# Kernel tuning notes

Measured on AMD Instinct MI355X. Metric: run time of the kernel, lower is better.

Reference implementation:

```python
import jax, jax.numpy as jnp
import numpy as np

B, C, H, W, K = 32, 64, 112, 112, 5


def setup_inputs() -> dict:
    key = jax.random.key(0)
    kx, = jax.random.split(key, 1)
    x = jax.random.uniform(kx, (B, C, H, W), dtype=jnp.float32)
    # parameters per BioNorm.reset_parameters()
    sigma = jnp.ones((C,), jnp.float32)
    pow_p = jnp.full((C,), 2.0, jnp.float32)
    sum_kernel = jnp.full((C, 1, K, K), 1.0 / (K * K), jnp.float32)
    weight = jnp.ones((C,), jnp.float32)
    bias = jnp.zeros((C,), jnp.float32)
    return {"x": x, "sigma": sigma, "pow_p": pow_p, "sum_kernel": sum_kernel,
            "weight": weight, "bias": bias}


def _bionorm(x, sigma, pow_p, sum_kernel, weight, bias):
    s = sigma.reshape(1, -1, 1, 1)
    p = pow_p.reshape(1, -1, 1, 1)
    w = weight.reshape(1, -1, 1, 1)
    b = bias.reshape(1, -1, 1, 1)
    xp = x ** p  # [B,C,H,W]
    # depthwise (grouped) conv, VALID padding -> [B,C,H-K+1,W-K+1]
    sf = jax.lax.conv_general_dilated(
        xp, sum_kernel, window_strides=(1, 1), padding='VALID',
        feature_group_count=C,
        dimension_numbers=('NCHW', 'OIHW', 'NCHW'))
    hks = K // 2
    # replicate-pad back to [B,C,H,W]
    sf = jnp.pad(sf, ((0, 0), (0, 0), (hks, hks), (hks, hks)), mode='edge')
    den = s ** p + sf
    return w * xp / den + b


def reference(x, sigma, pow_p, sum_kernel, weight, bias):
    return _bionorm(x, sigma, pow_p, sum_kernel, weight, bias)
```

## Files before the change

kernel.cpp:

```cpp
#include <hip/hip_runtime.h>


#define Cch 64
#define Hh 112
#define Ww 112
#define TH 28
#define LROWS (TH + 4)
#define ST 116

__global__ __launch_bounds__(256) void bionorm_kernel(
    const float* __restrict__ x, const float* __restrict__ sigma,
    const float* __restrict__ pow_p, const float* __restrict__ sum_kernel,
    const float* __restrict__ weight, const float* __restrict__ bias,
    float* __restrict__ out)
{
    __shared__ float lds[LROWS * ST];

    const int rt  = blockIdx.x;
    const int c   = blockIdx.y;
    const int b   = blockIdx.z;
    const int tid = threadIdx.x;
    const int r0  = rt * TH;

    const float p  = pow_p[c];
    const float sg = sigma[c];
    const float wc = weight[c];
    const float bc = bias[c];
    const bool  p2 = (p == 2.0f);
    const float sp = p2 ? sg * sg : __powf(sg, p);

    float kw[25];
    const float* kp = sum_kernel + c * 25;
    #pragma unroll
    for (int j = 0; j < 25; ++j) kw[j] = kp[j];

    const float* xplane = x + ((size_t)(b * Cch + c)) * Hh * Ww;

    for (int i = tid; i < LROWS * 28; i += 256) {
        int s = i / 28, q = i - s * 28;
        int g = r0 - 2 + s;
        g = g < 0 ? 0 : (g > 111 ? 111 : g);
        const float4 v = *(const float4*)(xplane + g * Ww + q * 4);
        float4 xp;
        if (p2) {
            xp.x = v.x * v.x; xp.y = v.y * v.y;
            xp.z = v.z * v.z; xp.w = v.w * v.w;
        } else {
            xp.x = __powf(v.x, p); xp.y = __powf(v.y, p);
            xp.z = __powf(v.z, p); xp.w = __powf(v.w, p);
        }
        *(float4*)(&lds[s * ST + q * 4]) = xp;
    }
    __syncthreads();

    float* oplane = out + ((size_t)(b * Cch + c)) * Hh * Ww;

    for (int i = tid; i < TH * 28; i += 256) {
        int lr = i / 28, gq = i - lr * 28;
        int r  = r0 + lr;
        int w0 = gq * 4;

        int cr    = r  < 2 ? 2 : (r  > 109 ? 109 : r);
        int cwmin = w0 < 2 ? 2 : (w0 > 109 ? 109 : w0);
        int base  = cwmin - 2;
        int sRow  = cr - r0;

        float S0 = 0.f, S1 = 0.f, S2 = 0.f, S3 = 0.f;
        #pragma unroll
        for (int dy = 0; dy < 5; ++dy) {
            const float* row = &lds[(sRow + dy) * ST + base];
            float rv[8];
            #pragma unroll
            for (int t = 0; t < 8; ++t) rv[t] = row[t];
            #pragma unroll
            for (int dx = 0; dx < 5; ++dx) {
                float kv = kw[dy * 5 + dx];
                S0 = fmaf(kv, rv[dx + 0], S0);
                S1 = fmaf(kv, rv[dx + 1], S1);
                S2 = fmaf(kv, rv[dx + 2], S2);
                S3 = fmaf(kv, rv[dx + 3], S3);
            }
        }

        const float4 xp4 = *(const float4*)(&lds[(lr + 2) * ST + w0]);
        const float xv[4] = {xp4.x, xp4.y, xp4.z, xp4.w};

        float res[4];
        #pragma unroll
        for (int j = 0; j < 4; ++j) {
            int wj  = w0 + j;
            int cwj = wj < 2 ? 2 : (wj > 109 ? 109 : wj);
            int off = cwj - cwmin;
            float s_ = off == 0 ? S0 : off == 1 ? S1 : off == 2 ? S2 : S3;
            res[j] = fmaf(wc * xv[j], __builtin_amdgcn_rcpf(sp + s_), bc);
        }
        float4 o = {res[0], res[1], res[2], res[3]};
        *(float4*)(oplane + r * Ww + w0) = o;
    }
}

extern "C" void kernel_launch(void* const* d_in, const int* in_sizes, int n_in,
                              void* d_out, int out_size, void* d_ws, size_t ws_size,
                              hipStream_t stream) {
    const float* x          = (const float*)d_in[0];
    const float* sigma      = (const float*)d_in[1];
    const float* pow_p      = (const float*)d_in[2];
    const float* sum_kernel = (const float*)d_in[3];
    const float* weight     = (const float*)d_in[4];
    const float* bias       = (const float*)d_in[5];
    float* out = (float*)d_out;

    dim3 grid(4, Cch, 32);
    dim3 block(256);
    bionorm_kernel<<<grid, block, 0, stream>>>(x, sigma, pow_p, sum_kernel,
                                               weight, bias, out);
}
```

Before: 214.7 us.

## Replace LDS tiling with register sliding-window stencil, shuffles, and uniform-kernel box-sum path

The kernel is restructured so each block handles a whole (b,c) plane. Each half-wave takes a 14-row band, and lanes keep a rolling 5-row window of powered values in registers. Horizontal neighbours come from lane shuffles instead of shared memory, and outputs use nontemporal stores. When all 25 kernel weights are equal, a running-sum box filter replaces the 25 FMAs, with a generic fallback for other weights. The intent is to remove LDS traffic, barriers and redundant halo loads, at the cost of fewer blocks and idle lanes (4 of every 32).

```diff
diff --git a/kernel.cpp b/kernel.cpp
--- a/kernel.cpp
+++ b/kernel.cpp
@@ -4,9 +4,8 @@
 #define Cch 64
 #define Hh 112
 #define Ww 112
-#define TH 28
-#define LROWS (TH + 4)
-#define ST 116
+
+typedef float v4f __attribute__((ext_vector_type(4)));
 
 __global__ __launch_bounds__(256) void bionorm_kernel(
     const float* __restrict__ x, const float* __restrict__ sigma,
@@ -14,13 +13,21 @@
     const float* __restrict__ weight, const float* __restrict__ bias,
     float* __restrict__ out)
 {
-    __shared__ float lds[LROWS * ST];
-
-    const int rt  = blockIdx.x;
-    const int c   = blockIdx.y;
-    const int b   = blockIdx.z;
-    const int tid = threadIdx.x;
-    const int r0  = rt * TH;
+    const int c    = blockIdx.x;
+    const int b    = blockIdx.y;
+    const int tid  = threadIdx.x;
+    const int wid  = tid >> 6;
+    const int lane = tid & 63;
+    const int half = lane >> 5;
+    const int li   = lane & 31;
+    if (li >= 28) return;
+
+    const int hb     = wid * 2 + half;
+    const int cstart = (hb == 0) ? 2 : 14 * hb;
+    const int ncent  = (hb == 0 || hb == 7) ? 12 : 14;
+    const int col0   = 4 * li;
+    const bool L0 = (li == 0), L27 = (li == 27);
+    const int laneL = lane - 1, laneR = lane + 1;
 
     const float p  = pow_p[c];
     const float sg = sigma[c];
@@ -29,74 +36,163 @@
     const bool  p2 = (p == 2.0f);
     const float sp = p2 ? sg * sg : __powf(sg, p);
 
+    const float* kp = sum_kernel + c * 25;
     float kw[25];
-    const float* kp = sum_kernel + c * 25;
     #pragma unroll
     for (int j = 0; j < 25; ++j) kw[j] = kp[j];
-
-    const float* xplane = x + ((size_t)(b * Cch + c)) * Hh * Ww;
-
-    for (int i = tid; i < LROWS * 28; i += 256) {
-        int s = i / 28, q = i - s * 28;
-        int g = r0 - 2 + s;
-        g = g < 0 ? 0 : (g > 111 ? 111 : g);
-        const float4 v = *(const float4*)(xplane + g * Ww + q * 4);
-        float4 xp;
-        if (p2) {
-            xp.x = v.x * v.x; xp.y = v.y * v.y;
-            xp.z = v.z * v.z; xp.w = v.w * v.w;
-        } else {
-            xp.x = __powf(v.x, p); xp.y = __powf(v.y, p);
-            xp.z = __powf(v.z, p); xp.w = __powf(v.w, p);
+    bool uni = true;
+    #pragma unroll
+    for (int j = 1; j < 25; ++j) uni = uni && (kw[j] == kw[0]);
+
+    const float* xplane = x + ((size_t)(b * Cch + c)) * (Hh * Ww);
+    float* oplane = out + ((size_t)(b * Cch + c)) * (Hh * Ww);
+
+    #define LOADR(GR) (*(const v4f*)(xplane + (GR) * Ww + col0))
+    const v4f r0 = LOADR(cstart - 2);
+    const v4f r1 = LOADR(cstart - 1);
+    const v4f r2 = LOADR(cstart    );
+    const v4f r3 = LOADR(cstart + 1);
+    v4f pend[2];
+    pend[0] = LOADR(cstart + 2);
+    pend[1] = LOADR(cstart + 3);
+
+    #define P4(V) (p2 ? (V) * (V) \
+        : (v4f){__powf((V).x, p), __powf((V).y, p), __powf((V).z, p), __powf((V).w, p)})
+
+    #define NTST(PTR, VAL) __builtin_nontemporal_store((VAL), (v4f*)(PTR))
+
+    if (uni) {
+        const float k0 = kw[0];
+        v4f xp[5];
+        xp[0] = P4(r0); xp[1] = P4(r1); xp[2] = P4(r2); xp[3] = P4(r3);
+        v4f vs = xp[0] + xp[1] + xp[2] + xp[3];
+
+        #pragma unroll
+        for (int k = 0; k < 14; ++k) {
+            const v4f nw = P4(pend[k & 1]);
+            xp[(k + 4) % 5] = nw;
+            vs += nw;
+            int lr = cstart + 4 + k; if (lr > 111) lr = 111;
+            pend[k & 1] = LOADR(lr);
+
+            const float vs0 = vs.x, vs1 = vs.y, vs2 = vs.z, vs3 = vs.w;
+            const float vL2 = __shfl(vs2, laneL, 64);
+            const float vL3 = __shfl(vs3, laneL, 64);
+            const float vR0 = __shfl(vs0, laneR, 64);
+            const float vR1 = __shfl(vs1, laneR, 64);
+            const float a  = vs0 + vs1 + vs2;
+            float h0 = vL2 + vL3 + a;
+            float h1 = vL3 + a + vs3;
+            float h2 = a + vs3 + vR0;
+            float h3 = (vs1 + vs2 + vs3) + (vR0 + vR1);
+            if (L0)  { h0 = h2; h1 = h2; }
+            if (L27) { h2 = h1; h3 = h1; }
+
+            const float d0 = __builtin_amdgcn_rcpf(fmaf(k0, h0, sp));
+            const float d1 = __builtin_amdgcn_rcpf(fmaf(k0, h1, sp));
+            const float d2 = __builtin_amdgcn_rcpf(fmaf(k0, h2, sp));
+            const float d3 = __builtin_amdgcn_rcpf(fmaf(k0, h3, sp));
+
+            const v4f nm = xp[(k + 2) % 5];
+            const v4f o  = {fmaf(wc * nm.x, d0, bc), fmaf(wc * nm.y, d1, bc),
+                            fmaf(wc * nm.z, d2, bc), fmaf(wc * nm.w, d3, bc)};
+            if (k < ncent)
+                NTST(oplane + (cstart + k) * Ww + col0, o);
+
+            if (hb == 0 && k == 0) {
+                const v4f nA = xp[0], nB = xp[1];
+                NTST(oplane + 0 * Ww + col0,
+                     ((v4f){fmaf(wc*nA.x,d0,bc), fmaf(wc*nA.y,d1,bc),
+                            fmaf(wc*nA.z,d2,bc), fmaf(wc*nA.w,d3,bc)}));
+                NTST(oplane + 1 * Ww + col0,
+                     ((v4f){fmaf(wc*nB.x,d0,bc), fmaf(wc*nB.y,d1,bc),
+                            fmaf(wc*nB.z,d2,bc), fmaf(wc*nB.w,d3,bc)}));
+            }
+            if (hb == 7 && k == 11) {
+                const v4f nA = xp[4];
+                const v4f nB = xp[0];
+                NTST(oplane + 110 * Ww + col0,
+                     ((v4f){fmaf(wc*nA.x,d0,bc), fmaf(wc*nA.y,d1,bc),
+                            fmaf(wc*nA.z,d2,bc), fmaf(wc*nA.w,d3,bc)}));
+                NTST(oplane + 111 * Ww + col0,
+                     ((v4f){fmaf(wc*nB.x,d0,bc), fmaf(wc*nB.y,d1,bc),
+                            fmaf(wc*nB.z,d2,bc), fmaf(wc*nB.w,d3,bc)}));
+            }
+
+            vs -= xp[k % 5];
         }
-        *(float4*)(&lds[s * ST + q * 4]) = xp;
+    } else {
+        float va[5][8];
+        #define CVT8G(SL, RV) { \
+            const v4f t_ = P4(RV); \
+            va[SL][2] = t_.x; va[SL][3] = t_.y; va[SL][4] = t_.z; va[SL][5] = t_.w; \
+            va[SL][0] = __shfl(t_.z, laneL, 64); \
+            va[SL][1] = __shfl(t_.w, laneL, 64); \
+            va[SL][6] = __shfl(t_.x, laneR, 64); \
+            va[SL][7] = __shfl(t_.y, laneR, 64); }
+
+        CVT8G(0, r0) CVT8G(1, r1) CVT8G(2, r2) CVT8G(3, r3)
+
+        #pragma unroll
+        for (int k = 0; k < 14; ++k) {
+            CVT8G((k + 4) % 5, pend[k & 1])
+            int lr = cstart + 4 + k; if (lr > 111) lr = 111;
+            pend[k & 1] = LOADR(lr);
+
+            float S0 = 0.f, S1 = 0.f, S2 = 0.f, S3 = 0.f;
+            #pragma unroll
+            for (int dy = 0; dy < 5; ++dy) {
+                const int sl = (k + dy) % 5;
+                #pragma unroll
+                for (int dx = 0; dx < 5; ++dx) {
+                    const float kv = kw[dy * 5 + dx];
+                    S0 = fmaf(kv, va[sl][dx + 0], S0);
+                    S1 = fmaf(kv, va[sl][dx + 1], S1);
+                    S2 = fmaf(kv, va[sl][dx + 2], S2);
+                    S3 = fmaf(kv, va[sl][dx + 3], S3);
+                }
+            }
+            if (L0)  { S0 = S2; S1 = S2; }
+            if (L27) { S2 = S1; S3 = S1; }
+
+            const float d0 = __builtin_amdgcn_rcpf(sp + S0);
+            const float d1 = __builtin_amdgcn_rcpf(sp + S1);
+            const float d2 = __builtin_amdgcn_rcpf(sp + S2);
+            const float d3 = __builtin_amdgcn_rcpf(sp + S3);
+
+            #define NUM4(SL) ((v4f){va[SL][2], va[SL][3], va[SL][4], va[SL][5]})
+            const v4f nm = NUM4((k + 2) % 5);
+            const v4f o  = {fmaf(wc * nm.x, d0, bc), fmaf(wc * nm.y, d1, bc),
+                            fmaf(wc * nm.z, d2, bc), fmaf(wc * nm.w, d3, bc)};
+            if (k < ncent)
+                NTST(oplane + (cstart + k) * Ww + col0, o);
+
+            if (hb == 0 && k == 0) {
+                const v4f nA = NUM4(0), nB = NUM4(1);
+                NTST(oplane + 0 * Ww + col0,
+                     ((v4f){fmaf(wc*nA.x,d0,bc), fmaf(wc*nA.y,d1,bc),
+                            fmaf(wc*nA.z,d2,bc), fmaf(wc*nA.w,d3,bc)}));
+                NTST(oplane + 1 * Ww + col0,
+                     ((v4f){fmaf(wc*nB.x,d0,bc), fmaf(wc*nB.y,d1,bc),
+                            fmaf(wc*nB.z,d2,bc), fmaf(wc*nB.w,d3,bc)}));
+            }
+            if (hb == 7 && k == 11) {
+                const v4f nA = NUM4(4);
+                const v4f nB = NUM4(0);
+                NTST(oplane + 110 * Ww + col0,
+                     ((v4f){fmaf(wc*nA.x,d0,bc), fmaf(wc*nA.y,d1,bc),
+                            fmaf(wc*nA.z,d2,bc), fmaf(wc*nA.w,d3,bc)}));
+                NTST(oplane + 111 * Ww + col0,
+                     ((v4f){fmaf(wc*nB.x,d0,bc), fmaf(wc*nB.y,d1,bc),
+                            fmaf(wc*nB.z,d2,bc), fmaf(wc*nB.w,d3,bc)}));
+            }
+            #undef NUM4
+        }
+        #undef CVT8G
     }
-    __syncthreads();
-
-    float* oplane = out + ((size_t)(b * Cch + c)) * Hh * Ww;
-
-    for (int i = tid; i < TH * 28; i += 256) {
-        int lr = i / 28, gq = i - lr * 28;
-        int r  = r0 + lr;
-        int w0 = gq * 4;
-
-        int cr    = r  < 2 ? 2 : (r  > 109 ? 109 : r);
-        int cwmin = w0 < 2 ? 2 : (w0 > 109 ? 109 : w0);
-        int base  = cwmin - 2;
-        int sRow  = cr - r0;
-
-        float S0 = 0.f, S1 = 0.f, S2 = 0.f, S3 = 0.f;
-        #pragma unroll
-        for (int dy = 0; dy < 5; ++dy) {
-            const float* row = &lds[(sRow + dy) * ST + base];
-            float rv[8];
-            #pragma unroll
-            for (int t = 0; t < 8; ++t) rv[t] = row[t];
-            #pragma unroll
-            for (int dx = 0; dx < 5; ++dx) {
-                float kv = kw[dy * 5 + dx];
-                S0 = fmaf(kv, rv[dx + 0], S0);
-                S1 = fmaf(kv, rv[dx + 1], S1);
-                S2 = fmaf(kv, rv[dx + 2], S2);
-                S3 = fmaf(kv, rv[dx + 3], S3);
-            }
-        }
-
-        const float4 xp4 = *(const float4*)(&lds[(lr + 2) * ST + w0]);
-        const float xv[4] = {xp4.x, xp4.y, xp4.z, xp4.w};
-
-        float res[4];
-        #pragma unroll
-        for (int j = 0; j < 4; ++j) {
-            int wj  = w0 + j;
-            int cwj = wj < 2 ? 2 : (wj > 109 ? 109 : wj);
-            int off = cwj - cwmin;
-            float s_ = off == 0 ? S0 : off == 1 ? S1 : off == 2 ? S2 : S3;
-            res[j] = fmaf(wc * xv[j], __builtin_amdgcn_rcpf(sp + s_), bc);
-        }
-        float4 o = {res[0], res[1], res[2], res[3]};
-        *(float4*)(oplane + r * Ww + w0) = o;
-    }
+    #undef P4
+    #undef NTST
+    #undef LOADR
 }
 
 extern "C" void kernel_launch(void* const* d_in, const int* in_sizes, int n_in,
@@ -110,7 +206,7 @@
     const float* bias       = (const float*)d_in[5];
     float* out = (float*)d_out;
 
-    dim3 grid(4, Cch, 32);
+    dim3 grid(Cch, 32);
     dim3 block(256);
     bionorm_kernel<<<grid, block, 0, stream>>>(x, sigma, pow_p, sum_kernel,
                                                weight, bias, out);
```

Measured after the change: 195.7 us. 1.1x faster.
